# Performance work log

Measured on AMD Instinct MI355X. Metric: run time of the kernel, lower is better.

The kernel has to match this reference:

```python
import jax, jax.numpy as jnp
import numpy as np

VOCAB = 100000
EMBED = 128
HIDDEN = 256
N_TRIPLES = 1_000_000


def setup_inputs() -> dict:
    key = jax.random.key(0)
    ks = jax.random.split(key, 12)

    def xavier(k, fan_in, fan_out):
        limit = float(np.sqrt(6.0 / (fan_in + fan_out)))
        return jax.random.uniform(k, (fan_in, fan_out), jnp.float32, -limit, limit)

    triples = jax.random.randint(ks[0], (N_TRIPLES, 3), 0, VOCAB, dtype=jnp.int32)
    entity_table = jax.random.normal(ks[1], (VOCAB, EMBED), jnp.float32) * 0.02
    relation_table = jax.random.normal(ks[2], (VOCAB, EMBED), jnp.float32) * 0.02
    return {
        "triples": triples,
        "entity_table": entity_table,
        "relation_table": relation_table,
        "W1": xavier(ks[3], 3 * EMBED, HIDDEN), "b1": jnp.zeros((HIDDEN,), jnp.float32),
        "W2": xavier(ks[4], HIDDEN, HIDDEN),    "b2": jnp.zeros((HIDDEN,), jnp.float32),
        "W3": xavier(ks[5], HIDDEN, EMBED),     "b3": jnp.zeros((EMBED,), jnp.float32),
        "Wf1": xavier(ks[6], EMBED, HIDDEN),    "bf1": jnp.zeros((HIDDEN,), jnp.float32),
        "Wf2": xavier(ks[7], HIDDEN, EMBED),    "bf2": jnp.zeros((EMBED,), jnp.float32),
    }


def reference(triples, entity_table, relation_table,
              W1, b1, W2, b2, W3, b3, Wf1, bf1, Wf2, bf2):
    # Batched gather: [N, embed] each
    e1 = entity_table[triples[:, 0]]
    rel = relation_table[triples[:, 1]]
    e2 = entity_table[triples[:, 2]]
    x = jnp.concatenate([e1, rel, e2], axis=-1)  # [N, 3*embed]
    # graph_encoder: Linear-ReLU-Linear-ReLU-Linear
    h = jax.nn.relu(x @ W1 + b1)
    h = jax.nn.relu(h @ W2 + b2)
    enc = h @ W3 + b3                            # [N, embed]
    agg = jnp.mean(enc, axis=0)                  # [embed]
    # final_encoder: Linear-ReLU-Linear
    out = jax.nn.relu(agg @ Wf1 + bf1) @ Wf2 + bf2
    return out
```

## Files before the change

kernel.cpp:

```cpp
#include <hip/hip_runtime.h>
#include <hip/hip_bf16.h>


#define EMBED 128
#define BM 64
#define NBUCKET 128

typedef __bf16 bf16x8 __attribute__((ext_vector_type(8)));
typedef __bf16 bf16x4 __attribute__((ext_vector_type(4)));
typedef float f32x4 __attribute__((ext_vector_type(4)));

__global__ void pack_cvt(const float* __restrict__ src, __bf16* __restrict__ dst,
                         int K, int N) {
    int e = blockIdx.x * 256 + threadIdx.x;
    if (e >= K * N) return;
    int j = e & 7;
    int l = (e >> 3) & 63;
    int tile = e >> 9;
    int KT = K >> 5;
    int kt = tile % KT;
    int mt = tile / KT;
    int k = kt * 32 + (l >> 4) * 8 + j;
    int nc = mt * 16 + (l & 15);
    dst[e] = (__bf16)src[k * N + nc];
}

__global__ __launch_bounds__(256, 3) void mlp_main(
    const int* __restrict__ triples,
    const float* __restrict__ ent, const float* __restrict__ rel,
    const __bf16* __restrict__ W1p, const float* __restrict__ b1,
    const __bf16* __restrict__ W2p, const float* __restrict__ b2,
    const __bf16* __restrict__ W3p,
    float* __restrict__ part, int n)
{
    __shared__ unsigned char lds[49152];
    unsigned char* xs  = lds;
    unsigned char* h1s = lds;
    unsigned char* h2s = lds;

    const int tid  = threadIdx.x;
    const int wave = tid >> 6;
    const int lane = tid & 63;
    const int l15  = lane & 15;
    const int l4   = lane >> 4;
    const int s0   = blockIdx.x * BM;
    const int sp   = tid >> 4;
    const int ch   = tid & 15;

    int rows[3][4];
#pragma unroll
    for (int p = 0; p < 4; p++) {
        int g = s0 + p * 16 + sp;
        const int* t = triples + (g < n ? g : 0) * 3;
        rows[0][p] = t[0]; rows[1][p] = t[1]; rows[2][p] = t[2];
    }
    float4 ga[3][4], gb[3][4];
#pragma unroll
    for (int c = 0; c < 3; c++) {
        const float* tbl = (c == 1) ? rel : ent;
#pragma unroll
        for (int p = 0; p < 4; p++) {
            const float* src = tbl + (long)rows[c][p] * EMBED + ch * 8;
            ga[c][p] = *(const float4*)src;
            gb[c][p] = *(const float4*)(src + 4);
        }
    }
#pragma unroll
    for (int c = 0; c < 3; c++)
#pragma unroll
        for (int p = 0; p < 4; p++) {
            bf16x8 w;
            w[0] = (__bf16)ga[c][p].x; w[1] = (__bf16)ga[c][p].y;
            w[2] = (__bf16)ga[c][p].z; w[3] = (__bf16)ga[c][p].w;
            w[4] = (__bf16)gb[c][p].x; w[5] = (__bf16)gb[c][p].y;
            w[6] = (__bf16)gb[c][p].z; w[7] = (__bf16)gb[c][p].w;
            int s = p * 16 + sp;
            int off = (s * 768 + c * 256 + ch * 16) ^ ((s & 7) << 4);
            *(bf16x8*)(xs + off) = w;
        }
    __syncthreads();

    f32x4 acc[4][4];
    {
        const int fb = wave * 64;
#pragma unroll
        for (int m = 0; m < 4; m++) {
            f32x4 bias = *(const f32x4*)(b1 + fb + m * 16 + l4 * 4);
#pragma unroll
            for (int nn = 0; nn < 4; nn++) acc[m][nn] = bias;
        }
    }
    __builtin_amdgcn_s_setprio(1);
#pragma unroll
    for (int kk = 0; kk < 12; kk++) {
        bf16x8 bfr[4];
#pragma unroll
        for (int nn = 0; nn < 4; nn++) {
            int s = nn * 16 + l15;
            int off = (s * 768 + kk * 64 + l4 * 16) ^ ((s & 7) << 4);
            bfr[nn] = *(const bf16x8*)(xs + off);
        }
        bf16x8 afr[4];
#pragma unroll
        for (int m = 0; m < 4; m++)
            afr[m] = *(const bf16x8*)(W1p + ((wave * 4 + m) * 12 + kk) * 512 + lane * 8);
#pragma unroll
        for (int m = 0; m < 4; m++)
#pragma unroll
            for (int nn = 0; nn < 4; nn++)
                acc[m][nn] = __builtin_amdgcn_mfma_f32_16x16x32_bf16(
                    afr[m], bfr[nn], acc[m][nn], 0, 0, 0);
    }
    __builtin_amdgcn_s_setprio(0);
    __syncthreads();
#pragma unroll
    for (int m = 0; m < 4; m++) {
        int f0 = wave * 64 + m * 16 + l4 * 4;
#pragma unroll
        for (int nn = 0; nn < 4; nn++) {
            int s = nn * 16 + l15;
            bf16x4 p;
#pragma unroll
            for (int j = 0; j < 4; j++) {
                float v = acc[m][nn][j];
                p[j] = (__bf16)(v > 0.f ? v : 0.f);
            }
            int off = (s * 512 + f0 * 2) ^ ((s & 7) << 4);
            *(bf16x4*)(h1s + off) = p;
        }
    }
    __syncthreads();

    f32x4 acc2[4][4];
    {
        const int fb = wave * 64;
#pragma unroll
        for (int m = 0; m < 4; m++) {
            f32x4 bias = *(const f32x4*)(b2 + fb + m * 16 + l4 * 4);
#pragma unroll
            for (int nn = 0; nn < 4; nn++) acc2[m][nn] = bias;
        }
    }
    __builtin_amdgcn_s_setprio(1);
#pragma unroll
    for (int kk = 0; kk < 8; kk++) {
        bf16x8 bfr[4];
#pragma unroll
        for (int nn = 0; nn < 4; nn++) {
            int s = nn * 16 + l15;
            int off = (s * 512 + kk * 64 + l4 * 16) ^ ((s & 7) << 4);
            bfr[nn] = *(const bf16x8*)(h1s + off);
        }
        bf16x8 afr[4];
#pragma unroll
        for (int m = 0; m < 4; m++)
            afr[m] = *(const bf16x8*)(W2p + ((wave * 4 + m) * 8 + kk) * 512 + lane * 8);
#pragma unroll
        for (int m = 0; m < 4; m++)
#pragma unroll
            for (int nn = 0; nn < 4; nn++)
                acc2[m][nn] = __builtin_amdgcn_mfma_f32_16x16x32_bf16(
                    afr[m], bfr[nn], acc2[m][nn], 0, 0, 0);
    }
    __builtin_amdgcn_s_setprio(0);
    __syncthreads();
#pragma unroll
    for (int m = 0; m < 4; m++) {
        int f0 = wave * 64 + m * 16 + l4 * 4;
#pragma unroll
        for (int nn = 0; nn < 4; nn++) {
            int s = nn * 16 + l15;
            bf16x4 p;
#pragma unroll
            for (int j = 0; j < 4; j++) {
                float v = acc2[m][nn][j];
                p[j] = (__bf16)(v > 0.f ? v : 0.f);
            }
            int off = (s * 512 + f0 * 2) ^ ((s & 7) << 4);
            *(bf16x4*)(h2s + off) = p;
        }
    }
    __syncthreads();

    f32x4 acc3[2][4];
#pragma unroll
    for (int m = 0; m < 2; m++)
#pragma unroll
        for (int nn = 0; nn < 4; nn++)
            acc3[m][nn] = (f32x4)(0.f);
    __builtin_amdgcn_s_setprio(1);
#pragma unroll
    for (int kk = 0; kk < 8; kk++) {
        bf16x8 bfr[4];
#pragma unroll
        for (int nn = 0; nn < 4; nn++) {
            int s = nn * 16 + l15;
            int off = (s * 512 + kk * 64 + l4 * 16) ^ ((s & 7) << 4);
            bfr[nn] = *(const bf16x8*)(h2s + off);
        }
        bf16x8 afr[2];
#pragma unroll
        for (int m = 0; m < 2; m++)
            afr[m] = *(const bf16x8*)(W3p + ((wave * 2 + m) * 8 + kk) * 512 + lane * 8);
#pragma unroll
        for (int m = 0; m < 2; m++)
#pragma unroll
            for (int nn = 0; nn < 4; nn++)
                acc3[m][nn] = __builtin_amdgcn_mfma_f32_16x16x32_bf16(
                    afr[m], bfr[nn], acc3[m][nn], 0, 0, 0);
    }
    __builtin_amdgcn_s_setprio(0);
    {
        float* bucket = part + (blockIdx.x & (NBUCKET - 1)) * 128;
#pragma unroll
        for (int m = 0; m < 2; m++) {
#pragma unroll
            for (int j = 0; j < 4; j++) {
                float v = 0.f;
#pragma unroll
                for (int nn = 0; nn < 4; nn++) {
                    int g = s0 + nn * 16 + l15;
                    float t = acc3[m][nn][j];
                    v += (g < n) ? t : 0.f;
                }
                for (int off = 1; off < 16; off <<= 1) v += __shfl_xor(v, off);
                if (l15 == 0) {
                    int f = wave * 32 + m * 16 + l4 * 4 + j;
                    atomicAdd(bucket + f, v);
                }
            }
        }
    }
}

__global__ void head_kernel(const float* __restrict__ part, const float* __restrict__ b3,
                            const float* __restrict__ Wf1, const float* __restrict__ bf1,
                            const float* __restrict__ Wf2, const float* __restrict__ bf2,
                            float* __restrict__ out, int n)
{
    __shared__ float agg[128];
    __shared__ float t[256];
    const int tid = threadIdx.x;
    if (tid < 128) {
        float s = 0.f;
        for (int b = 0; b < NBUCKET; b++) s += part[b * 128 + tid];
        agg[tid] = s / (float)n + b3[tid];
    }
    __syncthreads();
    {
        float a = bf1[tid];
        for (int k = 0; k < 128; k++) a += agg[k] * Wf1[k * 256 + tid];
        t[tid] = a > 0.f ? a : 0.f;
    }
    __syncthreads();
    if (tid < 128) {
        float o = bf2[tid];
        for (int i = 0; i < 256; i++) o += t[i] * Wf2[i * 128 + tid];
        out[tid] = o;
    }
}

extern "C" void kernel_launch(void* const* d_in, const int* in_sizes, int n_in,
                              void* d_out, int out_size, void* d_ws, size_t ws_size,
                              hipStream_t stream) {
    const int*   triples = (const int*)d_in[0];
    const float* ent     = (const float*)d_in[1];
    const float* rel     = (const float*)d_in[2];
    const float* W1      = (const float*)d_in[3];
    const float* b1      = (const float*)d_in[4];
    const float* W2      = (const float*)d_in[5];
    const float* b2      = (const float*)d_in[6];
    const float* W3      = (const float*)d_in[7];
    const float* b3      = (const float*)d_in[8];
    const float* Wf1     = (const float*)d_in[9];
    const float* bf1     = (const float*)d_in[10];
    const float* Wf2     = (const float*)d_in[11];
    const float* bf2     = (const float*)d_in[12];
    float* out = (float*)d_out;
    const int n = in_sizes[0] / 3;

    __bf16* W1p = (__bf16*)d_ws;
    __bf16* W2p = (__bf16*)((char*)d_ws + 196608);
    __bf16* W3p = (__bf16*)((char*)d_ws + 327680);
    float*  prt = (float*)((char*)d_ws + 393216);

    pack_cvt<<<(384 * 256 + 255) / 256, 256, 0, stream>>>(W1, W1p, 384, 256);
    pack_cvt<<<(256 * 256 + 255) / 256, 256, 0, stream>>>(W2, W2p, 256, 256);
    pack_cvt<<<(256 * 128 + 255) / 256, 256, 0, stream>>>(W3, W3p, 256, 128);
    hipMemsetAsync(prt, 0, NBUCKET * 128 * sizeof(float), stream);

    const int blocks = (n + BM - 1) / BM;
    mlp_main<<<blocks, 256, 0, stream>>>(triples, ent, rel, W1p, b1, W2p, b2, W3p, prt, n);
    head_kernel<<<1, 256, 0, stream>>>(prt, b3, Wf1, bf1, Wf2, bf2, out, n);
}
```

Baseline: 508.2 us.

## Halve row tile to 32, raise occupancy, merge weight prep launches

Shrinks the per-block row tile from 64 to 32, which halves the LDS footprint and the accumulator registers, and raises the launch bound to 4 blocks per CU. The gather is restructured so each group of 8 threads loads one full row, and the LDS swizzle gains an extra bit. The three weight-packing kernels and the memset are merged into one prep kernel to cut launch overhead. The trade-off is that each weight fragment loaded from global memory now feeds half as many MFMAs, so weight traffic per row doubles.

```diff
diff --git a/kernel.cpp b/kernel.cpp
--- a/kernel.cpp
+++ b/kernel.cpp
@@ -3,29 +3,34 @@
 
 
 #define EMBED 128
-#define BM 64
+#define BM 32
 #define NBUCKET 128
+#define SWZ(s) ((((s) & 7) << 4) ^ (((s) & 8) << 3))
 
 typedef __bf16 bf16x8 __attribute__((ext_vector_type(8)));
 typedef __bf16 bf16x4 __attribute__((ext_vector_type(4)));
 typedef float f32x4 __attribute__((ext_vector_type(4)));
 
-__global__ void pack_cvt(const float* __restrict__ src, __bf16* __restrict__ dst,
-                         int K, int N) {
-    int e = blockIdx.x * 256 + threadIdx.x;
-    if (e >= K * N) return;
-    int j = e & 7;
-    int l = (e >> 3) & 63;
-    int tile = e >> 9;
+__global__ void prep_all(const float* __restrict__ W1, const float* __restrict__ W2,
+                         const float* __restrict__ W3,
+                         __bf16* __restrict__ W1p, __bf16* __restrict__ W2p,
+                         __bf16* __restrict__ W3p, float* __restrict__ prt) {
+    int idx = blockIdx.x * 256 + threadIdx.x;
+    if (idx < NBUCKET * 128) prt[idx] = 0.f;
+    const float* src; __bf16* dst; int K, N, e;
+    if (idx < 98304)       { src = W1; dst = W1p; K = 384; N = 256; e = idx; }
+    else if (idx < 163840) { src = W2; dst = W2p; K = 256; N = 256; e = idx - 98304; }
+    else if (idx < 196608) { src = W3; dst = W3p; K = 256; N = 128; e = idx - 163840; }
+    else return;
+    int j = e & 7, l = (e >> 3) & 63, t = e >> 9;
     int KT = K >> 5;
-    int kt = tile % KT;
-    int mt = tile / KT;
-    int k = kt * 32 + (l >> 4) * 8 + j;
+    int kt = t % KT, mt = t / KT;
+    int k  = kt * 32 + (l >> 4) * 8 + j;
     int nc = mt * 16 + (l & 15);
     dst[e] = (__bf16)src[k * N + nc];
 }
 
-__global__ __launch_bounds__(256, 3) void mlp_main(
+__global__ __launch_bounds__(256, 4) void mlp_main(
     const int* __restrict__ triples,
     const float* __restrict__ ent, const float* __restrict__ rel,
     const __bf16* __restrict__ W1p, const float* __restrict__ b1,
@@ -33,7 +38,7 @@
     const __bf16* __restrict__ W3p,
     float* __restrict__ part, int n)
 {
-    __shared__ unsigned char lds[49152];
+    __shared__ unsigned char lds[24576];
     unsigned char* xs  = lds;
     unsigned char* h1s = lds;
     unsigned char* h2s = lds;
@@ -44,60 +49,53 @@
     const int l15  = lane & 15;
     const int l4   = lane >> 4;
     const int s0   = blockIdx.x * BM;
-    const int sp   = tid >> 4;
-    const int ch   = tid & 15;
-
-    int rows[3][4];
-#pragma unroll
-    for (int p = 0; p < 4; p++) {
-        int g = s0 + p * 16 + sp;
-        const int* t = triples + (g < n ? g : 0) * 3;
-        rows[0][p] = t[0]; rows[1][p] = t[1]; rows[2][p] = t[2];
-    }
-    float4 ga[3][4], gb[3][4];
-#pragma unroll
-    for (int c = 0; c < 3; c++) {
-        const float* tbl = (c == 1) ? rel : ent;
-#pragma unroll
-        for (int p = 0; p < 4; p++) {
-            const float* src = tbl + (long)rows[c][p] * EMBED + ch * 8;
-            ga[c][p] = *(const float4*)src;
-            gb[c][p] = *(const float4*)(src + 4);
-        }
-    }
-#pragma unroll
-    for (int c = 0; c < 3; c++)
-#pragma unroll
-        for (int p = 0; p < 4; p++) {
-            bf16x8 w;
-            w[0] = (__bf16)ga[c][p].x; w[1] = (__bf16)ga[c][p].y;
-            w[2] = (__bf16)ga[c][p].z; w[3] = (__bf16)ga[c][p].w;
-            w[4] = (__bf16)gb[c][p].x; w[5] = (__bf16)gb[c][p].y;
-            w[6] = (__bf16)gb[c][p].z; w[7] = (__bf16)gb[c][p].w;
-            int s = p * 16 + sp;
-            int off = (s * 768 + c * 256 + ch * 16) ^ ((s & 7) << 4);
-            *(bf16x8*)(xs + off) = w;
-        }
-    __syncthreads();
-
-    f32x4 acc[4][4];
+    const int srow = tid >> 3;
+    const int q    = tid & 7;
+
     {
-        const int fb = wave * 64;
-#pragma unroll
-        for (int m = 0; m < 4; m++) {
-            f32x4 bias = *(const f32x4*)(b1 + fb + m * 16 + l4 * 4);
-#pragma unroll
-            for (int nn = 0; nn < 4; nn++) acc[m][nn] = bias;
-        }
+        int g = s0 + srow;
+        const int* tp = triples + (long)(g < n ? g : 0) * 3;
+        float4 v[3][4];
+#pragma unroll
+        for (int c = 0; c < 3; c++) {
+            const float* tbl = (c == 1) ? rel : ent;
+            const float* src = tbl + (long)tp[c] * EMBED + q * 16;
+#pragma unroll
+            for (int i = 0; i < 4; i++) v[c][i] = *(const float4*)(src + i * 4);
+        }
+        const int swz = SWZ(srow);
+#pragma unroll
+        for (int c = 0; c < 3; c++) {
+#pragma unroll
+            for (int h = 0; h < 2; h++) {
+                bf16x8 w;
+#pragma unroll
+                for (int j = 0; j < 4; j++) {
+                    w[j]     = (__bf16)v[c][h * 2][j];
+                    w[j + 4] = (__bf16)v[c][h * 2 + 1][j];
+                }
+                int off = (srow * 768 + c * 256 + q * 32 + h * 16) ^ swz;
+                *(bf16x8*)(xs + off) = w;
+            }
+        }
+    }
+    __syncthreads();
+
+    f32x4 acc[4][2];
+#pragma unroll
+    for (int m = 0; m < 4; m++) {
+        f32x4 bias = *(const f32x4*)(b1 + wave * 64 + m * 16 + l4 * 4);
+#pragma unroll
+        for (int nn = 0; nn < 2; nn++) acc[m][nn] = bias;
     }
     __builtin_amdgcn_s_setprio(1);
 #pragma unroll
     for (int kk = 0; kk < 12; kk++) {
-        bf16x8 bfr[4];
-#pragma unroll
-        for (int nn = 0; nn < 4; nn++) {
-            int s = nn * 16 + l15;
-            int off = (s * 768 + kk * 64 + l4 * 16) ^ ((s & 7) << 4);
+        bf16x8 bfr[2];
+#pragma unroll
+        for (int nn = 0; nn < 2; nn++) {
+            int s = nn * 16 + l15;
+            int off = (s * 768 + kk * 64 + l4 * 16) ^ SWZ(s);
             bfr[nn] = *(const bf16x8*)(xs + off);
         }
         bf16x8 afr[4];
@@ -107,7 +105,7 @@
 #pragma unroll
         for (int m = 0; m < 4; m++)
 #pragma unroll
-            for (int nn = 0; nn < 4; nn++)
+            for (int nn = 0; nn < 2; nn++)
                 acc[m][nn] = __builtin_amdgcn_mfma_f32_16x16x32_bf16(
                     afr[m], bfr[nn], acc[m][nn], 0, 0, 0);
     }
@@ -117,7 +115,7 @@
     for (int m = 0; m < 4; m++) {
         int f0 = wave * 64 + m * 16 + l4 * 4;
 #pragma unroll
-        for (int nn = 0; nn < 4; nn++) {
+        for (int nn = 0; nn < 2; nn++) {
             int s = nn * 16 + l15;
             bf16x4 p;
 #pragma unroll
@@ -125,30 +123,27 @@
                 float v = acc[m][nn][j];
                 p[j] = (__bf16)(v > 0.f ? v : 0.f);
             }
-            int off = (s * 512 + f0 * 2) ^ ((s & 7) << 4);
+            int off = (s * 512 + f0 * 2) ^ SWZ(s);
             *(bf16x4*)(h1s + off) = p;
         }
     }
     __syncthreads();
 
-    f32x4 acc2[4][4];
-    {
-        const int fb = wave * 64;
-#pragma unroll
-        for (int m = 0; m < 4; m++) {
-            f32x4 bias = *(const f32x4*)(b2 + fb + m * 16 + l4 * 4);
-#pragma unroll
-            for (int nn = 0; nn < 4; nn++) acc2[m][nn] = bias;
-        }
+    f32x4 acc2[4][2];
+#pragma unroll
+    for (int m = 0; m < 4; m++) {
+        f32x4 bias = *(const f32x4*)(b2 + wave * 64 + m * 16 + l4 * 4);
+#pragma unroll
+        for (int nn = 0; nn < 2; nn++) acc2[m][nn] = bias;
     }
     __builtin_amdgcn_s_setprio(1);
 #pragma unroll
     for (int kk = 0; kk < 8; kk++) {
-        bf16x8 bfr[4];
-#pragma unroll
-        for (int nn = 0; nn < 4; nn++) {
-            int s = nn * 16 + l15;
-            int off = (s * 512 + kk * 64 + l4 * 16) ^ ((s & 7) << 4);
+        bf16x8 bfr[2];
+#pragma unroll
+        for (int nn = 0; nn < 2; nn++) {
+            int s = nn * 16 + l15;
+            int off = (s * 512 + kk * 64 + l4 * 16) ^ SWZ(s);
             bfr[nn] = *(const bf16x8*)(h1s + off);
         }
         bf16x8 afr[4];
@@ -158,7 +153,7 @@
 #pragma unroll
         for (int m = 0; m < 4; m++)
 #pragma unroll
-            for (int nn = 0; nn < 4; nn++)
+            for (int nn = 0; nn < 2; nn++)
                 acc2[m][nn] = __builtin_amdgcn_mfma_f32_16x16x32_bf16(
                     afr[m], bfr[nn], acc2[m][nn], 0, 0, 0);
     }
@@ -168,7 +163,7 @@
     for (int m = 0; m < 4; m++) {
         int f0 = wave * 64 + m * 16 + l4 * 4;
 #pragma unroll
-        for (int nn = 0; nn < 4; nn++) {
+        for (int nn = 0; nn < 2; nn++) {
             int s = nn * 16 + l15;
             bf16x4 p;
 #pragma unroll
@@ -176,26 +171,26 @@
                 float v = acc2[m][nn][j];
                 p[j] = (__bf16)(v > 0.f ? v : 0.f);
             }
-            int off = (s * 512 + f0 * 2) ^ ((s & 7) << 4);
+            int off = (s * 512 + f0 * 2) ^ SWZ(s);
             *(bf16x4*)(h2s + off) = p;
         }
     }
     __syncthreads();
 
-    f32x4 acc3[2][4];
+    f32x4 acc3[2][2];
 #pragma unroll
     for (int m = 0; m < 2; m++)
 #pragma unroll
-        for (int nn = 0; nn < 4; nn++)
+        for (int nn = 0; nn < 2; nn++)
             acc3[m][nn] = (f32x4)(0.f);
     __builtin_amdgcn_s_setprio(1);
 #pragma unroll
     for (int kk = 0; kk < 8; kk++) {
-        bf16x8 bfr[4];
-#pragma unroll
-        for (int nn = 0; nn < 4; nn++) {
-            int s = nn * 16 + l15;
-            int off = (s * 512 + kk * 64 + l4 * 16) ^ ((s & 7) << 4);
+        bf16x8 bfr[2];
+#pragma unroll
+        for (int nn = 0; nn < 2; nn++) {
+            int s = nn * 16 + l15;
+            int off = (s * 512 + kk * 64 + l4 * 16) ^ SWZ(s);
             bfr[nn] = *(const bf16x8*)(h2s + off);
         }
         bf16x8 afr[2];
@@ -205,7 +200,7 @@
 #pragma unroll
         for (int m = 0; m < 2; m++)
 #pragma unroll
-            for (int nn = 0; nn < 4; nn++)
+            for (int nn = 0; nn < 2; nn++)
                 acc3[m][nn] = __builtin_amdgcn_mfma_f32_16x16x32_bf16(
                     afr[m], bfr[nn], acc3[m][nn], 0, 0, 0);
     }
@@ -218,7 +213,7 @@
             for (int j = 0; j < 4; j++) {
                 float v = 0.f;
 #pragma unroll
-                for (int nn = 0; nn < 4; nn++) {
+                for (int nn = 0; nn < 2; nn++) {
                     int g = s0 + nn * 16 + l15;
                     float t = acc3[m][nn][j];
                     v += (g < n) ? t : 0.f;
@@ -284,10 +279,7 @@
     __bf16* W3p = (__bf16*)((char*)d_ws + 327680);
     float*  prt = (float*)((char*)d_ws + 393216);
 
-    pack_cvt<<<(384 * 256 + 255) / 256, 256, 0, stream>>>(W1, W1p, 384, 256);
-    pack_cvt<<<(256 * 256 + 255) / 256, 256, 0, stream>>>(W2, W2p, 256, 256);
-    pack_cvt<<<(256 * 128 + 255) / 256, 256, 0, stream>>>(W3, W3p, 256, 128);
-    hipMemsetAsync(prt, 0, NBUCKET * 128 * sizeof(float), stream);
+    prep_all<<<768, 256, 0, stream>>>(W1, W2, W3, W1p, W2p, W3p, prt);
 
     const int blocks = (n + BM - 1) / BM;
     mlp_main<<<blocks, 256, 0, stream>>>(triples, ent, rel, W1p, b1, W2p, b2, W3p, prt, n);
```

New measurement: 659.1 us. 29.7% more time.
